# Optimization experiments

Measured on AMD Instinct MI355X. Metric: run time of the kernel, lower is better.

## Reference

```python
import jax, jax.numpy as jnp
import numpy as np

CHUNKS = 4      # number of segments along in_features
QMAX = 127.0    # int8 symmetric fake quantization
EPS = 1e-8


def fake_quantize(t):
    """Per-tensor symmetric int8 fake quantization with amax scaling (STE-friendly)."""
    amax = jnp.max(jnp.abs(t))
    scale = jnp.maximum(amax / QMAX, EPS)
    q = jnp.clip(jnp.round(t / scale), -QMAX, QMAX) * scale
    # straight-through estimator: identity gradient through the quantizer
    return t + jax.lax.stop_gradient(q - t)


def setup_inputs() -> dict:
    key = jax.random.key(0)
    kx, kw = jax.random.split(key)
    N, K, O = 4096, 4096, 4096  # tokens (B*S), in_features, out_features
    x = jax.random.normal(kx, (N, K), dtype=jnp.float32)
    weight = jax.random.normal(kw, (O, K), dtype=jnp.float32)
    return {"x": x, "weight": weight}


def reference(x, weight):
    # seg_mode='input': split x and weight along in_features into CHUNKS equal chunks,
    # fake-quantize each chunk independently (per-chunk amax scale), run per-chunk
    # GEMMs y_i = fq(x_i) @ fq(w_i)^T and sum over chunks. No bias in 'input' mode.
    N, K = x.shape
    O = weight.shape[0]
    cs = K // CHUNKS
    xc = x.reshape(N, CHUNKS, cs)       # [N, C, cs]
    wc = weight.reshape(O, CHUNKS, cs)  # [O, C, cs]
    fq_chunks = jax.vmap(fake_quantize, in_axes=1, out_axes=1)  # independent amax per chunk
    xq = fq_chunks(xc)
    wq = fq_chunks(wc)
    # sum of per-chunk matmuls == contraction over (chunk, within-chunk) axes
    return jnp.einsum('nck,ock->no', xq, wq)
```

## Files before the change

kernel.cpp:

```cpp
#include <hip/hip_runtime.h>
#include <hip/hip_bf16.h>


constexpr int NDIM = 4096;
constexpr int TOTAL4 = (NDIM * NDIM) / 4;

typedef int i32x4 __attribute__((ext_vector_type(4)));

__global__ __launch_bounds__(256) void amax_kernel(
    const float* __restrict__ x, const float* __restrict__ w,
    unsigned int* __restrict__ amax) {
  const int t = threadIdx.x;
  const int c = blockIdx.x & 3;
  float mx = 0.f, mw = 0.f;
  const float4* x4 = (const float4*)x;
  const float4* w4 = (const float4*)w;
  const int stride = 1024 * 256;
  for (int i = blockIdx.x * 256 + t; i < TOTAL4; i += stride) {
    float4 v = x4[i];
    mx = fmaxf(mx, fmaxf(fmaxf(fabsf(v.x), fabsf(v.y)),
                         fmaxf(fabsf(v.z), fabsf(v.w))));
    float4 u = w4[i];
    mw = fmaxf(mw, fmaxf(fmaxf(fabsf(u.x), fabsf(u.y)),
                         fmaxf(fabsf(u.z), fabsf(u.w))));
  }
  __shared__ float r0[256], r1[256];
  r0[t] = mx; r1[t] = mw;
  __syncthreads();
  for (int off = 128; off; off >>= 1) {
    if (t < off) {
      r0[t] = fmaxf(r0[t], r0[t + off]);
      r1[t] = fmaxf(r1[t], r1[t + off]);
    }
    __syncthreads();
  }
  if (t == 0) {
    atomicMax(&amax[c],     __float_as_uint(r0[0]));
    atomicMax(&amax[4 + c], __float_as_uint(r1[0]));
  }
}

__device__ __forceinline__ signed char quant1(float v, float s) {
  float r = rintf(v / s);
  r = fminf(fmaxf(r, -127.f), 127.f);
  return (signed char)(int)r;
}

__global__ __launch_bounds__(256) void quant_kernel(
    const float* __restrict__ x, const float* __restrict__ w,
    const unsigned int* __restrict__ amax,
    signed char* __restrict__ qx, signed char* __restrict__ qw) {
  const int t = threadIdx.x;
  const int c = blockIdx.x & 3;
  const float sx = fmaxf(__uint_as_float(amax[c])     / 127.0f, 1e-8f);
  const float sw = fmaxf(__uint_as_float(amax[4 + c]) / 127.0f, 1e-8f);
  const float4* x4 = (const float4*)x;
  const float4* w4 = (const float4*)w;
  char4* qx4 = (char4*)qx;
  char4* qw4 = (char4*)qw;
  const int stride = 1024 * 256;
  for (int i = blockIdx.x * 256 + t; i < TOTAL4; i += stride) {
    float4 v = x4[i];
    char4 q;
    q.x = quant1(v.x, sx); q.y = quant1(v.y, sx);
    q.z = quant1(v.z, sx); q.w = quant1(v.w, sx);
    qx4[i] = q;
    float4 u = w4[i];
    char4 p;
    p.x = quant1(u.x, sw); p.y = quant1(u.y, sw);
    p.z = quant1(u.z, sw); p.w = quant1(u.w, sw);
    qw4[i] = p;
  }
}

__device__ __forceinline__ void async16(const void* g, void* l) {
  __builtin_amdgcn_global_load_lds(
      (const __attribute__((address_space(1))) void*)g,
      (__attribute__((address_space(3))) void*)l, 16, 0, 0);
}

__global__ __launch_bounds__(256, 2) void gemm_i8_kernel(
    const signed char* __restrict__ qx, const signed char* __restrict__ qw,
    const unsigned int* __restrict__ amax, float* __restrict__ out) {
  __shared__ __align__(1024) signed char lds_a[4][8192];
  __shared__ __align__(1024) signed char lds_b[4][8192];

  const int t = threadIdx.x;
  const int lane = t & 63;
  const int wave = t >> 6;
  const int brow = blockIdx.y * 128;
  const int bcol = blockIdx.x * 128;
  const int wr = wave >> 1;
  const int wc = wave & 1;

  const int ar0 = wave * 16 + (lane >> 2);
  const int ar1 = ar0 + 64;
  const int sl = lane & 3;
  const signed char* gax0 = qx + (size_t)(brow + ar0) * NDIM + ((sl ^ ((ar0 >> 1) & 3)) << 4);
  const signed char* gax1 = qx + (size_t)(brow + ar1) * NDIM + ((sl ^ ((ar1 >> 1) & 3)) << 4);
  const signed char* gbx0 = qw + (size_t)(bcol + ar0) * NDIM + ((sl ^ ((ar0 >> 1) & 3)) << 4);
  const signed char* gbx1 = qw + (size_t)(bcol + ar1) * NDIM + ((sl ^ ((ar1 >> 1) & 3)) << 4);
  const int ldsoff = wave * 1024;

  const int ra = wr * 64 + (lane & 15);
  const int rb = wc * 64 + (lane & 15);
  const int kg = lane >> 4;
  const int offa = ra * 64 + ((kg ^ ((ra >> 1) & 3)) << 4);
  const int offb = rb * 64 + ((kg ^ ((rb >> 1) & 3)) << 4);

#define STAGE(BUF, T)                                        \
  do {                                                       \
    const int kt_ = (T) * 64;                                \
    async16(gax0 + kt_, &lds_a[BUF][ldsoff]);                \
    async16(gax1 + kt_, &lds_a[BUF][ldsoff + 4096]);         \
    async16(gbx0 + kt_, &lds_b[BUF][ldsoff]);                \
    async16(gbx1 + kt_, &lds_b[BUF][ldsoff + 4096]);         \
  } while (0)

  STAGE(0, 0);
  STAGE(1, 1);
  STAGE(2, 2);

  const float s0 = fmaxf(__uint_as_float(amax[0]) / 127.0f, 1e-8f) *
                   fmaxf(__uint_as_float(amax[4]) / 127.0f, 1e-8f);
  const float s1 = fmaxf(__uint_as_float(amax[1]) / 127.0f, 1e-8f) *
                   fmaxf(__uint_as_float(amax[5]) / 127.0f, 1e-8f);
  const float s2 = fmaxf(__uint_as_float(amax[2]) / 127.0f, 1e-8f) *
                   fmaxf(__uint_as_float(amax[6]) / 127.0f, 1e-8f);
  const float s3 = fmaxf(__uint_as_float(amax[3]) / 127.0f, 1e-8f) *
                   fmaxf(__uint_as_float(amax[7]) / 127.0f, 1e-8f);

  i32x4 iacc[4][4];
  float facc[4][4][4];
#pragma unroll
  for (int m = 0; m < 4; ++m)
#pragma unroll
    for (int n = 0; n < 4; ++n) {
      iacc[m][n] = i32x4{0, 0, 0, 0};
#pragma unroll
      for (int j = 0; j < 4; ++j) facc[m][n][j] = 0.f;
    }

#define COMPUTE(BUF)                                                    \
  do {                                                                  \
    i32x4 av[4], bv[4];                                                 \
    _Pragma("unroll")                                                   \
    for (int m = 0; m < 4; ++m)                                         \
      av[m] = *(const i32x4*)&lds_a[BUF][offa + m * 1024];              \
    _Pragma("unroll")                                                   \
    for (int n = 0; n < 4; ++n)                                         \
      bv[n] = *(const i32x4*)&lds_b[BUF][offb + n * 1024];              \
    __builtin_amdgcn_s_setprio(1);                                      \
    _Pragma("unroll")                                                   \
    for (int m = 0; m < 4; ++m)                                         \
      _Pragma("unroll")                                                 \
      for (int n = 0; n < 4; ++n)                                       \
        iacc[m][n] = __builtin_amdgcn_mfma_i32_16x16x64_i8(             \
            av[m], bv[n], iacc[m][n], 0, 0, 0);                         \
    __builtin_amdgcn_s_setprio(0);                                      \
  } while (0)

#define FOLD(S)                                                         \
  do {                                                                  \
    _Pragma("unroll")                                                   \
    for (int m = 0; m < 4; ++m)                                         \
      _Pragma("unroll")                                                 \
      for (int n = 0; n < 4; ++n) {                                     \
        _Pragma("unroll")                                               \
        for (int j = 0; j < 4; ++j) facc[m][n][j] += (S) * (float)iacc[m][n][j]; \
        iacc[m][n] = i32x4{0, 0, 0, 0};                                 \
      }                                                                 \
  } while (0)

#define BODY(B)                                                          \
  do {                                                                   \
    const int t_ = t4 * 4 + (B);                                         \
    asm volatile("s_waitcnt vmcnt(8)" ::: "memory");                     \
    __builtin_amdgcn_sched_barrier(0);                                   \
    __builtin_amdgcn_s_barrier();                                        \
    __builtin_amdgcn_sched_barrier(0);                                   \
    COMPUTE(B);                                                          \
    asm volatile("s_waitcnt lgkmcnt(0)" ::: "memory");                   \
    __builtin_amdgcn_sched_barrier(0);                                   \
    __builtin_amdgcn_s_barrier();                                        \
    __builtin_amdgcn_sched_barrier(0);                                   \
    if ((B) == 0 || t4 < 15) STAGE(((B) + 3) & 3, t_ + 3);               \
    if (((B) & 3) == 3 && (t4 & 3) == 3) {                               \
      const int ci = t4 >> 2;                                            \
      const float sc_ = ci == 0 ? s0 : ci == 1 ? s1 : ci == 2 ? s2 : s3; \
      FOLD(sc_);                                                         \
    }                                                                    \
  } while (0)

#pragma unroll 1
  for (int t4 = 0; t4 < 16; ++t4) {
    BODY(0);
    BODY(1);
    BODY(2);
    BODY(3);
  }

  const int orow = brow + wr * 64 + (lane >> 4) * 4;
  const int ocol = bcol + wc * 64 + (lane & 15);
#pragma unroll
  for (int m = 0; m < 4; ++m)
#pragma unroll
    for (int n = 0; n < 4; ++n)
#pragma unroll
      for (int j = 0; j < 4; ++j)
        out[(size_t)(orow + m * 16 + j) * NDIM + (ocol + n * 16)] = facc[m][n][j];
#undef STAGE
#undef COMPUTE
#undef FOLD
#undef BODY
}

extern "C" void kernel_launch(void* const* d_in, const int* in_sizes, int n_in,
                              void* d_out, int out_size, void* d_ws, size_t ws_size,
                              hipStream_t stream) {
  const float* x = (const float*)d_in[0];
  const float* w = (const float*)d_in[1];
  float* out = (float*)d_out;

  unsigned int* amax = (unsigned int*)d_ws;
  signed char* qx = (signed char*)d_ws + 256;
  signed char* qw = qx + (size_t)NDIM * NDIM;

  hipMemsetAsync(d_ws, 0, 256, stream);
  amax_kernel<<<1024, 256, 0, stream>>>(x, w, amax);
  quant_kernel<<<1024, 256, 0, stream>>>(x, w, amax, qx, qw);
  dim3 grid(NDIM / 128, NDIM / 128);
  gemm_i8_kernel<<<grid, 256, 0, stream>>>(qx, qw, amax, out);
}
```

Measured before the change: 155.7 us.

## Switch int8 GEMM to double-buffered LDS for higher occupancy

Cuts the LDS ring for the int8 MFMA GEMM from four stages to two and raises the launch bound from 2 to 4 blocks per CU. The K loop is rewritten as an explicit ping-pong schedule with a peeled epilogue, and the per-chunk scale loads are hoisted ahead of the loop with a full vmcnt wait. The goal is more resident waves to hide global-load latency. The cost is a shallower prefetch distance and tighter register limits, which could cause spills with the 4x4 int and float accumulator arrays.

```diff
diff --git a/kernel.cpp b/kernel.cpp
--- a/kernel.cpp
+++ b/kernel.cpp
@@ -79,11 +79,11 @@
       (__attribute__((address_space(3))) void*)l, 16, 0, 0);
 }
 
-__global__ __launch_bounds__(256, 2) void gemm_i8_kernel(
+__global__ __launch_bounds__(256, 4) void gemm_i8_kernel(
     const signed char* __restrict__ qx, const signed char* __restrict__ qw,
     const unsigned int* __restrict__ amax, float* __restrict__ out) {
-  __shared__ __align__(1024) signed char lds_a[4][8192];
-  __shared__ __align__(1024) signed char lds_b[4][8192];
+  __shared__ __align__(1024) signed char lds_a[2][8192];
+  __shared__ __align__(1024) signed char lds_b[2][8192];
 
   const int t = threadIdx.x;
   const int lane = t & 63;
@@ -92,6 +92,17 @@
   const int bcol = blockIdx.x * 128;
   const int wr = wave >> 1;
   const int wc = wave & 1;
+
+  const float s0 = fmaxf(__uint_as_float(amax[0]) / 127.0f, 1e-8f) *
+                   fmaxf(__uint_as_float(amax[4]) / 127.0f, 1e-8f);
+  const float s1 = fmaxf(__uint_as_float(amax[1]) / 127.0f, 1e-8f) *
+                   fmaxf(__uint_as_float(amax[5]) / 127.0f, 1e-8f);
+  const float s2 = fmaxf(__uint_as_float(amax[2]) / 127.0f, 1e-8f) *
+                   fmaxf(__uint_as_float(amax[6]) / 127.0f, 1e-8f);
+  const float s3 = fmaxf(__uint_as_float(amax[3]) / 127.0f, 1e-8f) *
+                   fmaxf(__uint_as_float(amax[7]) / 127.0f, 1e-8f);
+  asm volatile("s_waitcnt vmcnt(0)" ::: "memory");
+  __builtin_amdgcn_sched_barrier(0);
 
   const int ar0 = wave * 16 + (lane >> 2);
   const int ar1 = ar0 + 64;
@@ -119,16 +130,6 @@
 
   STAGE(0, 0);
   STAGE(1, 1);
-  STAGE(2, 2);
-
-  const float s0 = fmaxf(__uint_as_float(amax[0]) / 127.0f, 1e-8f) *
-                   fmaxf(__uint_as_float(amax[4]) / 127.0f, 1e-8f);
-  const float s1 = fmaxf(__uint_as_float(amax[1]) / 127.0f, 1e-8f) *
-                   fmaxf(__uint_as_float(amax[5]) / 127.0f, 1e-8f);
-  const float s2 = fmaxf(__uint_as_float(amax[2]) / 127.0f, 1e-8f) *
-                   fmaxf(__uint_as_float(amax[6]) / 127.0f, 1e-8f);
-  const float s3 = fmaxf(__uint_as_float(amax[3]) / 127.0f, 1e-8f) *
-                   fmaxf(__uint_as_float(amax[7]) / 127.0f, 1e-8f);
 
   i32x4 iacc[4][4];
   float facc[4][4][4];
@@ -172,33 +173,38 @@
       }                                                                 \
   } while (0)
 
-#define BODY(B)                                                          \
-  do {                                                                   \
-    const int t_ = t4 * 4 + (B);                                         \
-    asm volatile("s_waitcnt vmcnt(8)" ::: "memory");                     \
-    __builtin_amdgcn_sched_barrier(0);                                   \
-    __builtin_amdgcn_s_barrier();                                        \
-    __builtin_amdgcn_sched_barrier(0);                                   \
-    COMPUTE(B);                                                          \
-    asm volatile("s_waitcnt lgkmcnt(0)" ::: "memory");                   \
-    __builtin_amdgcn_sched_barrier(0);                                   \
-    __builtin_amdgcn_s_barrier();                                        \
-    __builtin_amdgcn_sched_barrier(0);                                   \
-    if ((B) == 0 || t4 < 15) STAGE(((B) + 3) & 3, t_ + 3);               \
-    if (((B) & 3) == 3 && (t4 & 3) == 3) {                               \
-      const int ci = t4 >> 2;                                            \
-      const float sc_ = ci == 0 ? s0 : ci == 1 ? s1 : ci == 2 ? s2 : s3; \
-      FOLD(sc_);                                                         \
-    }                                                                    \
-  } while (0)
+#define WAITV(N) \
+  asm volatile("s_waitcnt vmcnt(" #N ")" ::: "memory"); \
+  __builtin_amdgcn_sched_barrier(0)
+#define WAITL \
+  asm volatile("s_waitcnt lgkmcnt(0)" ::: "memory"); \
+  __builtin_amdgcn_sched_barrier(0)
+#define BAR \
+  __builtin_amdgcn_s_barrier(); \
+  __builtin_amdgcn_sched_barrier(0)
 
 #pragma unroll 1
-  for (int t4 = 0; t4 < 16; ++t4) {
-    BODY(0);
-    BODY(1);
-    BODY(2);
-    BODY(3);
-  }
+  for (int it = 0; it < 31; ++it) {
+    WAITV(4); BAR;
+    COMPUTE(0);
+    WAITL; BAR;
+    STAGE(0, 2 * it + 2);
+    WAITV(4); BAR;
+    COMPUTE(1);
+    WAITL; BAR;
+    STAGE(1, 2 * it + 3);
+    if ((it & 7) == 7) {
+      const int ci = it >> 3;
+      const float sc_ = ci == 0 ? s0 : ci == 1 ? s1 : s2;
+      FOLD(sc_);
+    }
+  }
+  WAITV(4); BAR;
+  COMPUTE(0);
+  WAITL; BAR;
+  WAITV(0); BAR;
+  COMPUTE(1);
+  FOLD(s3);
 
   const int orow = brow + wr * 64 + (lane >> 4) * 4;
   const int ocol = bcol + wc * 64 + (lane & 15);
@@ -212,7 +218,9 @@
 #undef STAGE
 #undef COMPUTE
 #undef FOLD
-#undef BODY
+#undef WAITV
+#undef WAITL
+#undef BAR
 }
 
 extern "C" void kernel_launch(void* const* d_in, const int* in_sizes, int n_in,
```

Result: slower. 211.7 us (+35.9%).
